# Kernel optimization log

Hardware: AMD Instinct MI355X
Metric: run time of the kernel (lower is better)

The kernel has to match this reference:

```python
import jax, jax.numpy as jnp
import numpy as np

N, E = 100000, 1600000
DIM, H, D = 64, 4, 8          # dim, num_heads, qk_dim
DH = D * H                    # 32
QK_SCALE = (DIM // H) ** -0.5


def setup_inputs() -> dict:
    key = jax.random.key(0)
    k1, k2, k3, k4 = jax.random.split(key, 4)
    x = jax.random.normal(k1, (N, DIM), dtype=jnp.float32)
    edge_index = jax.random.randint(k2, (2, E), 0, N, dtype=jnp.int64)
    W_qkv = jax.random.normal(k3, (DIM, 2 * DH + DIM), dtype=jnp.float32) * (DIM ** -0.5)
    b_qkv = jax.random.normal(k4, (2 * DH + DIM,), dtype=jnp.float32) * 0.02
    return {"x": x, "edge_index": edge_index, "W_qkv": W_qkv, "b_qkv": b_qkv}


def reference(x, edge_index, W_qkv, b_qkv):
    n = x.shape[0]
    e = edge_index.shape[1]
    qkv = x @ W_qkv + b_qkv                       # (N, 2*DH+DIM)
    q = qkv[:, :DH].reshape(n, H, D)
    k = qkv[:, DH:2 * DH].reshape(n, H, D)
    v = qkv[:, 2 * DH:].reshape(n, H, DIM // H)
    s, t = edge_index[0], edge_index[1]
    q_e = q[s] * QK_SCALE                         # (E, H, D)
    k_e = k[t]
    v_e = v[t]                                    # (E, H, DIM/H)
    # scale q by 1/sqrt(num source neighbors) (bincount of s)
    deg = jax.ops.segment_sum(jnp.ones((e,), x.dtype), s, num_segments=n)
    q_e = q_e * (deg[s] ** -0.5)[:, None, None]
    compat = jnp.einsum('ehd,ehd->eh', q_e, k_e)  # (E, H)
    # segment softmax over edges grouped by source node s
    m = jax.ops.segment_max(compat, s, num_segments=n)
    ex = jnp.exp(compat - m[s])
    denom = jax.ops.segment_sum(ex, s, num_segments=n)
    attn = ex / (denom[s] + 1e-16)                # (E, H)
    msg = (v_e * attn[..., None]).reshape(e, DIM)  # (E, DIM)
    out = jax.ops.segment_sum(msg, s, num_segments=n)  # (N, DIM)
    return out
```

## Files before the change

kernel.cpp:

```cpp
#include <hip/hip_runtime.h>


#define NDIM 64
#define NBMAX 1024
#define CTILE 8192
#define STGMAX 4352
#define GEMM_BLKS 256

static __device__ __forceinline__ unsigned short f2bf(float f) {
    unsigned int u = __float_as_uint(f);
    unsigned int r = (u + 0x7fffu + ((u >> 16) & 1u)) >> 16;
    return (unsigned short)r;
}

__global__ void fused_bin_gemm_kernel(const int* __restrict__ s_arr,
                                      const int* __restrict__ t_arr,
                                      unsigned int* __restrict__ gcur,
                                      unsigned int* __restrict__ binned,
                                      const float* __restrict__ x,
                                      const float* __restrict__ W,
                                      const float* __restrict__ bvec,
                                      float* __restrict__ qs,
                                      unsigned short* __restrict__ kv,
                                      int N, int E, int nbin) {
    __shared__ unsigned int sm[12288];
    unsigned int* hist  = sm;
    unsigned int* off   = sm + 1024;
    unsigned int* gbase = sm + 2048;
    unsigned int* psum  = sm + 3072;
    unsigned int* stg   = sm + 4096;
    int tid = threadIdx.x;

    if (blockIdx.x < (unsigned)nbin) {
        int e0 = blockIdx.x * CTILE;
        int cnt = min(CTILE, E - e0);

        hist[tid] = 0;
        __syncthreads();
        for (int i = tid; i < cnt; i += 1024)
            atomicAdd(&hist[(unsigned)s_arr[e0 + i] >> 7], 1u);
        __syncthreads();

        unsigned int v = hist[tid];
        unsigned int acc = v;
        psum[tid] = acc;
        __syncthreads();
        for (int o = 1; o < 1024; o <<= 1) {
            unsigned int add = (tid >= o) ? psum[tid - o] : 0;
            __syncthreads();
            acc += add;
            psum[tid] = acc;
            __syncthreads();
        }
        off[tid] = acc - v;
        __syncthreads();

        for (int i = tid; i < cnt; i += 1024) {
            int s = s_arr[e0 + i];
            int t = t_arr[e0 + i];
            unsigned int bkt = (unsigned)s >> 7;
            unsigned int p = atomicAdd(&off[bkt], 1u);
            stg[p] = ((unsigned)(s & 127) << 17) | (unsigned)t;
        }
        __syncthreads();

        {
            unsigned int h = hist[tid];
            unsigned int resv = h ? atomicAdd(&gcur[tid], h) : 0u;
            unsigned int m = (resv < STGMAX) ? min(h, STGMAX - resv) : 0u;
            hist[tid] = m;
            gbase[tid] = (unsigned)tid * STGMAX + resv;
        }
        __syncthreads();

        int wid = tid >> 6, lane = tid & 63;
        for (int b = wid; b < NBMAX; b += 16) {
            unsigned int m = hist[b];
            if (m == 0) continue;
            unsigned int src = off[b] - ((off[b] - m) - (off[b] - m));
            unsigned int segstart = off[b];
            unsigned int start = (b > 0) ? psum[b - 1] : 0u;
            unsigned int dst = gbase[b];
            for (unsigned int i = lane; i < m; i += 64)
                binned[dst + i] = stg[start + i];
            (void)src; (void)segstart;
        }
    } else {
        float4* xs = (float4*)sm;
        int bid = blockIdx.x - nbin;
        int col = tid & 127;
        int rw  = tid >> 7;
        float w[64];
        #pragma unroll
        for (int k = 0; k < 64; ++k) w[k] = W[k * 128 + col];
        float bias = bvec[col];

        for (int r0 = bid * 8; r0 < N; r0 += GEMM_BLKS * 8) {
            __syncthreads();
            if (tid < 128) {
                int rr = tid >> 4;
                int cc = tid & 15;
                int n = r0 + rr;
                xs[rr * 16 + cc] = (n < N)
                    ? reinterpret_cast<const float4*>(x)[(size_t)n * 16 + cc]
                    : make_float4(0.f, 0.f, 0.f, 0.f);
            }
            __syncthreads();
            int n = r0 + rw;
            if (n < N) {
                float acc = bias;
                #pragma unroll
                for (int k4 = 0; k4 < 16; ++k4) {
                    float4 xv = xs[rw * 16 + k4];
                    acc = fmaf(xv.x, w[4 * k4 + 0], acc);
                    acc = fmaf(xv.y, w[4 * k4 + 1], acc);
                    acc = fmaf(xv.z, w[4 * k4 + 2], acc);
                    acc = fmaf(xv.w, w[4 * k4 + 3], acc);
                }
                if (col < 32) {
                    qs[(size_t)n * 32 + col] = acc;
                } else if (col < 64) {
                    kv[(size_t)n * 96 + (col - 32)] = f2bf(acc);
                } else {
                    kv[(size_t)n * 96 + 32 + (col - 64)] = f2bf(acc);
                }
            }
        }
    }
}

#define COMPUTE_EDGE(rr)                                              \
    {                                                                 \
        float lo = __uint_as_float((rr) << 16);                       \
        float hi = __uint_as_float((rr) & 0xffff0000u);               \
        float p = fmaf(q0, lo, q1 * hi);                              \
        p += __shfl_xor(p, 1);                                        \
        p += __shfl_xor(p, 2);                                        \
        float c = __shfl(p, csrc);                                    \
        float w = __expf(c);                                          \
        accx = fmaf(w, lo, accx);                                     \
        accy = fmaf(w, hi, accy);                                     \
        den += w;                                                     \
    }

__global__ void __launch_bounds__(512, 8)
sort_aggregate_kernel(const unsigned int* __restrict__ gcur,
                      const unsigned int* __restrict__ binned,
                      const float* __restrict__ qs,
                      const unsigned int* __restrict__ kv32,
                      float* __restrict__ out, int N) {
    __shared__ unsigned int hist[128];
    __shared__ unsigned int rstart[128];
    __shared__ unsigned int cur[128];
    __shared__ unsigned int sh[128];
    __shared__ unsigned int stg[STGMAX];

    int b = blockIdx.x;
    int tid = threadIdx.x;
    unsigned int base = (unsigned)b * STGMAX;
    unsigned int cnt = min(gcur[b], (unsigned int)STGMAX);

    if (tid < 128) hist[tid] = 0;
    __syncthreads();
    for (unsigned int i = tid; i < cnt; i += 512)
        atomicAdd(&hist[binned[base + i] >> 17], 1u);
    __syncthreads();

    unsigned int v = (tid < 128) ? hist[tid] : 0;
    unsigned int acc = v;
    if (tid < 128) sh[tid] = acc;
    __syncthreads();
    for (int o = 1; o < 128; o <<= 1) {
        unsigned int add = (tid >= o && tid < 128) ? sh[tid - o] : 0;
        __syncthreads();
        if (tid < 128) { acc += add; sh[tid] = acc; }
        __syncthreads();
    }
    if (tid < 128) {
        unsigned int exc = acc - v;
        rstart[tid] = exc;
        cur[tid] = exc;
    }
    __syncthreads();

    for (unsigned int i = tid; i < cnt; i += 512) {
        unsigned int e = binned[base + i];
        unsigned int p = atomicAdd(&cur[e >> 17], 1u);
        stg[p] = (e & 0x1FFFFu) * 192u;
    }
    __syncthreads();

    int wid = tid >> 6, lane = tid & 63;
    unsigned int lane4 = ((unsigned int)lane) << 2;
    bool ldact = (lane < 48);
    const char* kvb = (const char*)kv32;
    int csrc = (lane < 16) ? (lane & ~3)
             : (lane < 48) ? (((lane - 16) >> 3) << 2)
                           : 0;

    for (int nl = wid * 16; nl < wid * 16 + 16; ++nl) {
        int n = b * 128 + nl;
        if (n >= N) break;
        int dg = (int)hist[nl];
        if (dg == 0) {
            if (lane >= 16 && lane < 48)
                *reinterpret_cast<float2*>(&out[(size_t)n * 64 + 2 * (lane - 16)]) =
                    make_float2(0.f, 0.f);
            continue;
        }
        int start = (int)rstart[nl];
        float sc = 0.25f * rsqrtf((float)dg);
        float q0 = 0.f, q1 = 0.f;
        if (lane < 16) {
            q0 = qs[(size_t)n * 32 + 2 * lane] * sc;
            q1 = qs[(size_t)n * 32 + 2 * lane + 1] * sc;
        }

        float accx = 0.f, accy = 0.f, den = 0.f;
        int j = start;
        int rem = dg;

        unsigned int ra0 = 0, ra1 = 0, ra2 = 0, ra3 = 0;
        if (rem >= 4) {
            unsigned int o0 = stg[j] + lane4,     o1 = stg[j + 1] + lane4;
            unsigned int o2 = stg[j + 2] + lane4, o3 = stg[j + 3] + lane4;
            if (ldact) {
                ra0 = *(const unsigned int*)(kvb + o0);
                ra1 = *(const unsigned int*)(kvb + o1);
                ra2 = *(const unsigned int*)(kvb + o2);
                ra3 = *(const unsigned int*)(kvb + o3);
            }
        }
        while (rem >= 4) {
            unsigned int rb0 = 0, rb1 = 0, rb2 = 0, rb3 = 0;
            if (rem >= 8) {
                unsigned int o0 = stg[j + 4] + lane4, o1 = stg[j + 5] + lane4;
                unsigned int o2 = stg[j + 6] + lane4, o3 = stg[j + 7] + lane4;
                if (ldact) {
                    rb0 = *(const unsigned int*)(kvb + o0);
                    rb1 = *(const unsigned int*)(kvb + o1);
                    rb2 = *(const unsigned int*)(kvb + o2);
                    rb3 = *(const unsigned int*)(kvb + o3);
                }
            }
            COMPUTE_EDGE(ra0);
            COMPUTE_EDGE(ra1);
            COMPUTE_EDGE(ra2);
            COMPUTE_EDGE(ra3);
            ra0 = rb0; ra1 = rb1; ra2 = rb2; ra3 = rb3;
            j += 4; rem -= 4;
        }
        for (; rem > 0; --rem, ++j) {
            unsigned int o0 = stg[j] + lane4;
            unsigned int r0 = ldact ? *(const unsigned int*)(kvb + o0) : 0u;
            COMPUTE_EDGE(r0);
        }

        if (lane >= 16 && lane < 48) {
            float inv = 1.0f / (den + 1e-16f);
            float2 o = make_float2(accx * inv, accy * inv);
            *reinterpret_cast<float2*>(&out[(size_t)n * 64 + 2 * (lane - 16)]) = o;
        }
    }
}

extern "C" void kernel_launch(void* const* d_in, const int* in_sizes, int n_in,
                              void* d_out, int out_size, void* d_ws, size_t ws_size,
                              hipStream_t stream) {
    const float* x = (const float*)d_in[0];
    const int*   eidx = (const int*)d_in[1];
    const float* W = (const float*)d_in[2];
    const float* b = (const float*)d_in[3];
    int N = in_sizes[0] / NDIM;
    int E = in_sizes[1] / 2;
    float* out = (float*)d_out;

    int NB = (N + 127) / 128;
    int nbin = (E + CTILE - 1) / CTILE;

    float* qs = (float*)d_ws;
    unsigned short* kv = (unsigned short*)(qs + (size_t)N * 32);
    unsigned int* gcur = (unsigned int*)(kv + (size_t)N * 96);
    unsigned int* binned = gcur + NBMAX;

    const int* s_arr = eidx;
    const int* t_arr = eidx + E;

    hipMemsetAsync(gcur, 0, NBMAX * sizeof(unsigned int), stream);

    fused_bin_gemm_kernel<<<nbin + GEMM_BLKS, 1024, 0, stream>>>(
        s_arr, t_arr, gcur, binned, x, W, b, qs, kv, N, E, nbin);
    sort_aggregate_kernel<<<NB, 512, 0, stream>>>(
        gcur, binned, qs, (const unsigned int*)kv, out, N);
}
```

Baseline: 175.7 us.

## Process two edges per wavefront half and store queries as bf16

```diff
diff --git a/kernel.cpp b/kernel.cpp
--- a/kernel.cpp
+++ b/kernel.cpp
@@ -11,6 +11,12 @@
     unsigned int u = __float_as_uint(f);
     unsigned int r = (u + 0x7fffu + ((u >> 16) & 1u)) >> 16;
     return (unsigned short)r;
+}
+static __device__ __forceinline__ float bflo(unsigned int u) {
+    return __uint_as_float(u << 16);
+}
+static __device__ __forceinline__ float bfhi(unsigned int u) {
+    return __uint_as_float(u & 0xffff0000u);
 }
 
 __global__ void fused_bin_gemm_kernel(const int* __restrict__ s_arr,
@@ -20,7 +26,7 @@
                                       const float* __restrict__ x,
                                       const float* __restrict__ W,
                                       const float* __restrict__ bvec,
-                                      float* __restrict__ qs,
+                                      unsigned short* __restrict__ qs16,
                                       unsigned short* __restrict__ kv,
                                       int N, int E, int nbin) {
     __shared__ unsigned int sm[12288];
@@ -77,13 +83,10 @@
         for (int b = wid; b < NBMAX; b += 16) {
             unsigned int m = hist[b];
             if (m == 0) continue;
-            unsigned int src = off[b] - ((off[b] - m) - (off[b] - m));
-            unsigned int segstart = off[b];
             unsigned int start = (b > 0) ? psum[b - 1] : 0u;
             unsigned int dst = gbase[b];
             for (unsigned int i = lane; i < m; i += 64)
                 binned[dst + i] = stg[start + i];
-            (void)src; (void)segstart;
         }
     } else {
         float4* xs = (float4*)sm;
@@ -118,7 +121,7 @@
                     acc = fmaf(xv.w, w[4 * k4 + 3], acc);
                 }
                 if (col < 32) {
-                    qs[(size_t)n * 32 + col] = acc;
+                    qs16[(size_t)n * 32 + col] = f2bf(acc);
                 } else if (col < 64) {
                     kv[(size_t)n * 96 + (col - 32)] = f2bf(acc);
                 } else {
@@ -129,24 +132,10 @@
     }
 }
 
-#define COMPUTE_EDGE(rr)                                              \
-    {                                                                 \
-        float lo = __uint_as_float((rr) << 16);                       \
-        float hi = __uint_as_float((rr) & 0xffff0000u);               \
-        float p = fmaf(q0, lo, q1 * hi);                              \
-        p += __shfl_xor(p, 1);                                        \
-        p += __shfl_xor(p, 2);                                        \
-        float c = __shfl(p, csrc);                                    \
-        float w = __expf(c);                                          \
-        accx = fmaf(w, lo, accx);                                     \
-        accy = fmaf(w, hi, accy);                                     \
-        den += w;                                                     \
-    }
-
 __global__ void __launch_bounds__(512, 8)
 sort_aggregate_kernel(const unsigned int* __restrict__ gcur,
                       const unsigned int* __restrict__ binned,
-                      const float* __restrict__ qs,
+                      const unsigned short* __restrict__ qs16,
                       const unsigned int* __restrict__ kv32,
                       float* __restrict__ out, int N) {
     __shared__ unsigned int hist[128];
@@ -191,75 +180,73 @@
     __syncthreads();
 
     int wid = tid >> 6, lane = tid & 63;
-    unsigned int lane4 = ((unsigned int)lane) << 2;
-    bool ldact = (lane < 48);
+    int hl   = lane & 31;
+    int sub  = lane >> 5;
+    int head = hl >> 3;
     const char* kvb = (const char*)kv32;
-    int csrc = (lane < 16) ? (lane & ~3)
-             : (lane < 48) ? (((lane - 16) >> 3) << 2)
-                           : 0;
+    const char* qsb = (const char*)qs16;
 
     for (int nl = wid * 16; nl < wid * 16 + 16; ++nl) {
         int n = b * 128 + nl;
         if (n >= N) break;
         int dg = (int)hist[nl];
         if (dg == 0) {
-            if (lane >= 16 && lane < 48)
-                *reinterpret_cast<float2*>(&out[(size_t)n * 64 + 2 * (lane - 16)]) =
+            if (lane < 32)
+                *reinterpret_cast<float2*>(&out[(size_t)n * 64 + 2 * hl]) =
                     make_float2(0.f, 0.f);
             continue;
         }
         int start = (int)rstart[nl];
+        int last = start + dg - 1;
         float sc = 0.25f * rsqrtf((float)dg);
-        float q0 = 0.f, q1 = 0.f;
-        if (lane < 16) {
-            q0 = qs[(size_t)n * 32 + 2 * lane] * sc;
-            q1 = qs[(size_t)n * 32 + 2 * lane + 1] * sc;
-        }
+
+        uint4 q4 = *(const uint4*)(qsb + (size_t)n * 64 + (head << 4));
+        float qf0 = bflo(q4.x) * sc, qf1 = bfhi(q4.x) * sc;
+        float qf2 = bflo(q4.y) * sc, qf3 = bfhi(q4.y) * sc;
+        float qf4 = bflo(q4.z) * sc, qf5 = bfhi(q4.z) * sc;
+        float qf6 = bflo(q4.w) * sc, qf7 = bfhi(q4.w) * sc;
 
         float accx = 0.f, accy = 0.f, den = 0.f;
-        int j = start;
-        int rem = dg;
-
-        unsigned int ra0 = 0, ra1 = 0, ra2 = 0, ra3 = 0;
-        if (rem >= 4) {
-            unsigned int o0 = stg[j] + lane4,     o1 = stg[j + 1] + lane4;
-            unsigned int o2 = stg[j + 2] + lane4, o3 = stg[j + 3] + lane4;
-            if (ldact) {
-                ra0 = *(const unsigned int*)(kvb + o0);
-                ra1 = *(const unsigned int*)(kvb + o1);
-                ra2 = *(const unsigned int*)(kvb + o2);
-                ra3 = *(const unsigned int*)(kvb + o3);
+        int npairs = (dg + 1) >> 1;
+        int idx = start + sub;
+
+        unsigned int co = stg[min(idx, last)];
+        float wm = (idx <= last) ? 1.f : 0.f;
+        uint4 kr = *(const uint4*)(kvb + co + (head << 4));
+        unsigned int vr = *(const unsigned int*)(kvb + co + 64 + (hl << 2));
+
+        for (int i = 0; i < npairs; ++i) {
+            uint4 kr2 = kr; unsigned int vr2 = vr; float wm2 = 0.f;
+            int idx2 = idx + 2;
+            if (i + 1 < npairs) {
+                unsigned int co2 = stg[min(idx2, last)];
+                wm2 = (idx2 <= last) ? 1.f : 0.f;
+                kr2 = *(const uint4*)(kvb + co2 + (head << 4));
+                vr2 = *(const unsigned int*)(kvb + co2 + 64 + (hl << 2));
             }
-        }
-        while (rem >= 4) {
-            unsigned int rb0 = 0, rb1 = 0, rb2 = 0, rb3 = 0;
-            if (rem >= 8) {
-                unsigned int o0 = stg[j + 4] + lane4, o1 = stg[j + 5] + lane4;
-                unsigned int o2 = stg[j + 6] + lane4, o3 = stg[j + 7] + lane4;
-                if (ldact) {
-                    rb0 = *(const unsigned int*)(kvb + o0);
-                    rb1 = *(const unsigned int*)(kvb + o1);
-                    rb2 = *(const unsigned int*)(kvb + o2);
-                    rb3 = *(const unsigned int*)(kvb + o3);
-                }
-            }
-            COMPUTE_EDGE(ra0);
-            COMPUTE_EDGE(ra1);
-            COMPUTE_EDGE(ra2);
-            COMPUTE_EDGE(ra3);
-            ra0 = rb0; ra1 = rb1; ra2 = rb2; ra3 = rb3;
-            j += 4; rem -= 4;
-        }
-        for (; rem > 0; --rem, ++j) {
-            unsigned int o0 = stg[j] + lane4;
-            unsigned int r0 = ldact ? *(const unsigned int*)(kvb + o0) : 0u;
-            COMPUTE_EDGE(r0);
-        }
-
-        if (lane >= 16 && lane < 48) {
+            float p = qf0 * bflo(kr.x);
+            p = fmaf(qf1, bfhi(kr.x), p);
+            p = fmaf(qf2, bflo(kr.y), p);
+            p = fmaf(qf3, bfhi(kr.y), p);
+            p = fmaf(qf4, bflo(kr.z), p);
+            p = fmaf(qf5, bfhi(kr.z), p);
+            p = fmaf(qf6, bflo(kr.w), p);
+            p = fmaf(qf7, bfhi(kr.w), p);
+            float w = __expf(p) * wm;
+            accx = fmaf(w, bflo(vr), accx);
+            accy = fmaf(w, bfhi(vr), accy);
+            den += w;
+            kr = kr2; vr = vr2; wm = wm2; idx = idx2;
+        }
+
+        accx += __shfl_xor(accx, 32);
+        accy += __shfl_xor(accy, 32);
+        den  += __shfl_xor(den, 32);
+
+        if (lane < 32) {
             float inv = 1.0f / (den + 1e-16f);
-            float2 o = make_float2(accx * inv, accy * inv);
-            *reinterpret_cast<float2*>(&out[(size_t)n * 64 + 2 * (lane - 16)]) = o;
+            *reinterpret_cast<float2*>(&out[(size_t)n * 64 + 2 * hl]) =
+                make_float2(accx * inv, accy * inv);
         }
     }
 }
@@ -278,8 +265,8 @@
     int NB = (N + 127) / 128;
     int nbin = (E + CTILE - 1) / CTILE;
 
-    float* qs = (float*)d_ws;
-    unsigned short* kv = (unsigned short*)(qs + (size_t)N * 32);
+    unsigned short* qs16 = (unsigned short*)d_ws;
+    unsigned short* kv = qs16 + (size_t)N * 32;
     unsigned int* gcur = (unsigned int*)(kv + (size_t)N * 96);
     unsigned int* binned = gcur + NBMAX;
 
@@ -289,7 +276,7 @@
     hipMemsetAsync(gcur, 0, NBMAX * sizeof(unsigned int), stream);
 
     fused_bin_gemm_kernel<<<nbin + GEMM_BLKS, 1024, 0, stream>>>(
-        s_arr, t_arr, gcur, binned, x, W, b, qs, kv, N, E, nbin);
+        s_arr, t_arr, gcur, binned, x, W, b, qs16, kv, N, E, nbin);
     sort_aggregate_kernel<<<NB, 512, 0, stream>>>(
-        gcur, binned, qs, (const unsigned int*)kv, out, N);
-}
+        gcur, binned, qs16, (const unsigned int*)kv, out, N);
+}
```

Result: faster. 171.5 us, median of 2 (-2.4%).
